# Kernel tuning notes

Measured on AMD Instinct MI355X. Metric: run time of the kernel, lower is better.

## Reference

```python
import jax, jax.numpy as jnp
import numpy as np

B, S, E, H = 2, 2048, 1024, 16
D = E // H  # head_dim
SCALE = 1.0 / np.sqrt(D)


def rope_tables(seq_len, dim, dtype=jnp.float32):
    # matches RotaryEmbedding: inv_freq over even indices, emb = cat([freqs, freqs])
    inv_freq = 1.0 / (10000.0 ** (jnp.arange(0, dim, 2, dtype=dtype) / dim))
    t = jnp.arange(seq_len, dtype=dtype)
    freqs = t[:, None] * inv_freq[None, :]          # [S, D/2]
    emb = jnp.concatenate([freqs, freqs], axis=-1)  # [S, D]
    return jnp.cos(emb)[None, None], jnp.sin(emb)[None, None]  # [1,1,S,D]


def apply_rope(x, cos, sin):
    # x: [B,H,S,D]; interleaved rotate exactly as the torch code:
    # x2 = stack([-x[...,1::2], x[...,0::2]], -1).reshape_as(x)
    x2 = jnp.stack([-x[..., 1::2], x[..., 0::2]], axis=-1).reshape(x.shape)
    return x * cos + x2 * sin


def setup_inputs() -> dict:
    key = jax.random.key(0)
    ks = jax.random.split(key, 12)
    std = 1.0 / np.sqrt(E)
    inp = {
        "query": jax.random.normal(ks[0], (B, S, E), jnp.float32),
        "key": jax.random.normal(ks[1], (B, S, E), jnp.float32),
        "value": jax.random.normal(ks[2], (B, S, E), jnp.float32),
        "mask": jnp.ones((B, S), jnp.int32),
        "Wq": jax.random.normal(ks[3], (E, E), jnp.float32) * std,
        "bq": jax.random.normal(ks[4], (E,), jnp.float32) * std,
        "Wk": jax.random.normal(ks[5], (E, E), jnp.float32) * std,
        "bk": jax.random.normal(ks[6], (E,), jnp.float32) * std,
        "Wv": jax.random.normal(ks[7], (E, E), jnp.float32) * std,
        "bv": jax.random.normal(ks[8], (E,), jnp.float32) * std,
        "Wo": jax.random.normal(ks[9], (E, E), jnp.float32) * std,
        "bo": jax.random.normal(ks[10], (E,), jnp.float32) * std,
    }
    return inp


def reference(query, key, value, mask, Wq, bq, Wk, bk, Wv, bv, Wo, bo):
    b, sq, _ = query.shape
    sk = key.shape[1]
    # linear projections (torch Linear: x @ W.T + b), split into heads [B,H,S,D]
    Q = (query @ Wq.T + bq).reshape(b, sq, H, D).transpose(0, 2, 1, 3)
    K = (key @ Wk.T + bk).reshape(b, sk, H, D).transpose(0, 2, 1, 3)
    V = (value @ Wv.T + bv).reshape(b, sk, H, D).transpose(0, 2, 1, 3)
    cos_q, sin_q = rope_tables(sq, D)
    cos_k, sin_k = rope_tables(sk, D)
    Q = apply_rope(Q, cos_q, sin_q)
    K = apply_rope(K, cos_k, sin_k)
    scores = jnp.einsum("bhqd,bhkd->bhqk", Q, K) * SCALE
    neg_inf = jnp.finfo(scores.dtype).min
    scores = jnp.where(mask[:, None, None, :] == 0, neg_inf, scores)
    attn = jax.nn.softmax(scores, axis=-1)
    # dropout omitted (deterministic reference / eval mode)
    out = jnp.einsum("bhqk,bhkd->bhqd", attn, V)
    out = out.transpose(0, 2, 1, 3).reshape(b, sq, E)
    return out @ Wo.T + bo
```

## Files before the change

### kernel.cpp

```cpp
#include <hip/hip_runtime.h>
#include <stdint.h>

typedef unsigned short u16;
typedef __bf16 bf16x8 __attribute__((ext_vector_type(8)));
typedef float f32x4 __attribute__((ext_vector_type(4)));
typedef float f32x2 __attribute__((ext_vector_type(2)));
typedef u16 u16x4v __attribute__((ext_vector_type(4)));

#define DI __device__ __forceinline__

constexpr int BB = 2, SS = 2048, EE = 1024, HH = 16, DD = 64;
constexpr int MROWS = BB * SS;
constexpr int KDIM = 1024, NDIM = 1024;

DI u16 f2bf(float f) {
  uint32_t u = __float_as_uint(f);
  return (u16)((u + 0x7FFFu + ((u >> 16) & 1u)) >> 16);
}
DI float bf2f(u16 h) { return __uint_as_float(((uint32_t)h) << 16); }

DI uint32_t cvtpk_bf16(float a, float b) {
  uint32_t r;
  asm("v_cvt_pk_bf16_f32 %0, %1, %2" : "=v"(r) : "v"(a), "v"(b));
  return r;
}

DI void cp16(const void* g, void* lds) {
  __builtin_amdgcn_global_load_lds((const __attribute__((address_space(1))) void*)g,
                                   (__attribute__((address_space(3))) void*)lds, 16, 0, 0);
}

DI f32x4 mfma16(bf16x8 a, bf16x8 b, f32x4 c) {
  return __builtin_amdgcn_mfma_f32_16x16x32_bf16(a, b, c, 0, 0, 0);
}

__global__ __launch_bounds__(256) void prep_cast(
    const float* __restrict__ q, const float* __restrict__ k, const float* __restrict__ v,
    const float* __restrict__ wq, const float* __restrict__ wk, const float* __restrict__ wv,
    const float* __restrict__ wo,
    u16* __restrict__ qb, u16* __restrict__ kb, u16* __restrict__ vb,
    u16* __restrict__ wqb, u16* __restrict__ wkb, u16* __restrict__ wvb,
    u16* __restrict__ wob) {
  constexpr size_t SZI = (size_t)MROWS * EE;
  constexpr size_t SZW = (size_t)EE * EE;
  const size_t g = ((size_t)blockIdx.x * 256 + threadIdx.x) * 4;
  const float* src; u16* dst; size_t o;
  if (g < SZI)          { src = q; dst = qb; o = g; }
  else if (g < 2 * SZI) { src = k; dst = kb; o = g - SZI; }
  else if (g < 3 * SZI) { src = v; dst = vb; o = g - 2 * SZI; }
  else {
    size_t t2 = g - 3 * SZI;
    int wi = (int)(t2 / SZW);
    o = t2 - (size_t)(wi < 4 ? wi : 3) * SZW;
    src = wi == 0 ? wq : wi == 1 ? wk : wi == 2 ? wv : wo;
    dst = wi == 0 ? wqb : wi == 1 ? wkb : wi == 2 ? wvb : wob;
  }
  const float4 f = *(const float4*)(src + o);
  u16x4v hv;
  hv[0] = f2bf(f.x); hv[1] = f2bf(f.y); hv[2] = f2bf(f.z); hv[3] = f2bf(f.w);
  *(u16x4v*)(dst + o) = hv;
}

__global__ __launch_bounds__(256) void rope_tables_k(float* __restrict__ csT) {
  const int t = blockIdx.x * 256 + threadIdx.x;
  const int s = t >> 6, d = t & 63, j = d & 31;
  const float ang = (float)s * exp2f(-(float)j * 0.4152410118f);
  float2 cs; cs.x = cosf(ang); cs.y = sinf(ang);
  ((float2*)csT)[t] = cs;
}

__global__ __launch_bounds__(256) void gemm_qkv(
    const u16* __restrict__ qb, const u16* __restrict__ kb, const u16* __restrict__ vb,
    const u16* __restrict__ wqb, const u16* __restrict__ wkb, const u16* __restrict__ wvb,
    const float* __restrict__ bq, const float* __restrict__ bk, const float* __restrict__ bv,
    u16* __restrict__ Qp, u16* __restrict__ Kp, u16* __restrict__ Vtg,
    const float* __restrict__ csT) {
  __shared__ alignas(16) u16 sA[128 * 64];
  __shared__ alignas(16) u16 sB[128 * 64];
  const int tsel = blockIdx.y >> 5;
  const bool vtr = (tsel == 2);
  const u16* A    = tsel == 0 ? wqb : tsel == 1 ? wkb : vb;
  const u16* Bm   = tsel == 0 ? qb  : tsel == 1 ? kb  : wvb;
  const float* bias = tsel == 0 ? bq : tsel == 1 ? bk : bv;

  const int fBase = blockIdx.x * 128;
  const int tBase = (blockIdx.y & 31) * 128;
  const int aBase = vtr ? tBase : fBase;
  const int bBase = vtr ? fBase : tBase;
  const int tid = threadIdx.x;
  const int lane = tid & 63, w = tid >> 6;
  const int quad = lane >> 4, l16 = lane & 15;
  const int wr = w >> 1, wc = w & 1;

  size_t aSrc[4], bSrc[4];
  u16 *aDst[4], *bDst[4];
#pragma unroll
  for (int j = 0; j < 4; ++j) {
    const int c = tid + j * 256;
    const int row = c >> 3, sl = c & 7;
    const size_t off = (size_t)row * KDIM + ((sl ^ (row & 7)) * 8);
    aSrc[j] = (size_t)aBase * KDIM + off; aDst[j] = &sA[c * 8];
    bSrc[j] = (size_t)bBase * KDIM + off; bDst[j] = &sB[c * 8];
  }

  f32x4 acc[4][4];
#pragma unroll
  for (int mi = 0; mi < 4; ++mi)
#pragma unroll
    for (int ni = 0; ni < 4; ++ni)
#pragma unroll
      for (int e = 0; e < 4; ++e) acc[mi][ni][e] = 0.f;

  const int arow = wr * 64 + l16, brow = wc * 64 + l16;

  for (int k0 = 0; k0 < KDIM; k0 += 64) {
    __syncthreads();
#pragma unroll
    for (int j = 0; j < 4; ++j) {
      cp16(A + aSrc[j] + k0, aDst[j]);
      cp16(Bm + bSrc[j] + k0, bDst[j]);
    }
    __syncthreads();
#pragma unroll
    for (int h = 0; h < 2; ++h) {
      bf16x8 af[4], bf[4];
#pragma unroll
      for (int i = 0; i < 4; ++i) {
        const int ar = arow + i * 16, br = brow + i * 16;
        af[i] = *(const bf16x8*)&sA[ar * 64 + (((h * 4 + quad) ^ (ar & 7)) << 3)];
        bf[i] = *(const bf16x8*)&sB[br * 64 + (((h * 4 + quad) ^ (br & 7)) << 3)];
      }
#pragma unroll
      for (int mi = 0; mi < 4; ++mi)
#pragma unroll
        for (int ni = 0; ni < 4; ++ni)
          acc[mi][ni] = mfma16(af[mi], bf[ni], acc[mi][ni]);
    }
  }

  if (!vtr) {
    u16* C = tsel == 0 ? Qp : Kp;
#pragma unroll
    for (int mi = 0; mi < 4; ++mi) {
      const int fm = fBase + wr * 64 + mi * 16 + quad * 4;
      const float4 b4 = *(const float4*)&bias[fm];
      const int d0 = fm & 63;
#pragma unroll
      for (int ni = 0; ni < 4; ++ni) {
        const int t = tBase + wc * 64 + ni * 16 + l16;
        const int srow = t & (SS - 1);
        const float* cs = &csT[(size_t)((srow << 6) + d0) * 2];
        const float4 cs01 = *(const float4*)cs;
        const float4 cs23 = *(const float4*)(cs + 4);
        const float v0 = acc[mi][ni][0] + b4.x;
        const float v1 = acc[mi][ni][1] + b4.y;
        const float v2 = acc[mi][ni][2] + b4.z;
        const float v3 = acc[mi][ni][3] + b4.w;
        const float o0 = v0 * cs01.x - v1 * cs01.y;
        const float o1 = v1 * cs01.z + v0 * cs01.w;
        const float o2 = v2 * cs23.x - v3 * cs23.y;
        const float o3 = v3 * cs23.z + v2 * cs23.w;
        uint2 pk;
        pk.x = cvtpk_bf16(o0, o1);
        pk.y = cvtpk_bf16(o2, o3);
        *(uint2*)&C[(size_t)t * NDIM + fm] = pk;
      }
    }
  } else {
#pragma unroll
    for (int ni = 0; ni < 4; ++ni) {
      const int f = fBase + wc * 64 + ni * 16 + l16;
      const int h = f >> 6, d = f & 63;
      const float bb = bias[f];
#pragma unroll
      for (int mi = 0; mi < 4; ++mi) {
        const int t0 = tBase + wr * 64 + mi * 16 + quad * 4;
        const int b = t0 >> 11, s0 = t0 & (SS - 1);
        const int sp0 = (s0 & ~31) | (((s0 >> 2) & 3) << 3) | (((s0 >> 4) & 1) << 2);
        uint2 pk;
        pk.x = cvtpk_bf16(acc[mi][ni][0] + bb, acc[mi][ni][1] + bb);
        pk.y = cvtpk_bf16(acc[mi][ni][2] + bb, acc[mi][ni][3] + bb);
        *(uint2*)&Vtg[((size_t)((b * 16 + h) * 64 + d)) * SS + sp0] = pk;
      }
    }
  }
}

__global__ __launch_bounds__(512, 4) void attn_kernel(
    const u16* __restrict__ Qp, const u16* __restrict__ Kp, const u16* __restrict__ Vtg,
    const int* __restrict__ mask, u16* __restrict__ Oh) {
  __shared__ alignas(16) u16 sK[128 * 64];
  __shared__ alignas(16) u16 sVt[64 * 128];
  __shared__ float sMask[128];
  const int tid = threadIdx.x, lane = tid & 63, w = tid >> 6;
  const int quad = lane >> 4, l16 = lane & 15;
  const int bh = blockIdx.y, b = bh >> 4, h = bh & 15;
  const int q0 = blockIdx.x * 128 + w * 16;
  const u16* Qb = Qp + (size_t)b * SS * EE + h * DD;
  const u16* Kb = Kp + (size_t)b * SS * EE + h * DD;
  const u16* Vb = Vtg + (size_t)bh * DD * SS;
  constexpr float C1 = 0.18033688011112042f;
  constexpr float FM = 12.0f;
  constexpr float MNEG = -30000.f;

  bf16x8 qf[2];
#pragma unroll
  for (int ks = 0; ks < 2; ++ks)
    qf[ks] = *(const bf16x8*)(Qb + (size_t)(q0 + l16) * EE + ks * 32 + quad * 8);

  f32x4 oacc[4];
#pragma unroll
  for (int nd = 0; nd < 4; ++nd)
#pragma unroll
    for (int e = 0; e < 4; ++e) oacc[nd][e] = 0.f;
  f32x2 sum2 = {0.f, 0.f};

  for (int kt = 0; kt < SS / 128; ++kt) {
    const int key0 = kt * 128;
    __syncthreads();
#pragma unroll
    for (int i = 0; i < 2; ++i) {
      const int c = i * 512 + tid;
      const int key = c >> 3;
      const int g8 = ((c & 7) ^ (key & 7)) * 8;
      cp16(Kb + (size_t)(key0 + key) * EE + g8, &sK[c * 8]);
    }
#pragma unroll
    for (int i = 0; i < 2; ++i) {
      const int L = i * 512 + tid;
      const int d = L >> 4;
      const int g8 = ((L & 15) ^ (d & 15)) * 8;
      cp16(Vb + (size_t)d * SS + key0 + g8, &sVt[L * 8]);
    }
    if (tid < 128) sMask[tid] = mask[b * SS + key0 + tid] ? -FM : MNEG;
    __syncthreads();

    f32x4 sacc[8];
#pragma unroll
    for (int ni = 0; ni < 8; ++ni)
#pragma unroll
      for (int e = 0; e < 4; ++e) sacc[ni][e] = 0.f;
#pragma unroll
    for (int ks = 0; ks < 2; ++ks)
#pragma unroll
      for (int ni = 0; ni < 8; ++ni) {
        const int row = ni * 16 + l16;
        const bf16x8 kf = *(const bf16x8*)&sK[row * 64 + (((ks * 4 + quad) ^ (l16 & 7)) << 3)];
        sacc[ni] = mfma16(kf, qf[ks], sacc[ni]);
      }

    uint32_t pw32[4][4];
#pragma unroll
    for (int ni = 0; ni < 8; ++ni) {
      const int kb4 = ni * 16 + quad * 4;
      const f32x2 m01 = *(const f32x2*)&sMask[kb4];
      const f32x2 m23 = *(const f32x2*)&sMask[kb4 + 2];
      f32x2 t01, t23;
      t01.x = sacc[ni][0]; t01.y = sacc[ni][1];
      t23.x = sacc[ni][2]; t23.y = sacc[ni][3];
      t01 = t01 * C1 + m01;
      t23 = t23 * C1 + m23;
      f32x2 p01, p23;
      p01.x = exp2f(t01.x); p01.y = exp2f(t01.y);
      p23.x = exp2f(t23.x); p23.y = exp2f(t23.y);
      sum2 += p01;
      sum2 += p23;
      const int k2 = ni >> 1, j2 = (ni & 1) * 2;
      pw32[k2][j2]     = cvtpk_bf16(p01.x, p01.y);
      pw32[k2][j2 + 1] = cvtpk_bf16(p23.x, p23.y);
    }

#pragma unroll
    for (int k2 = 0; k2 < 4; ++k2) {
      union { uint32_t u[4]; bf16x8 v; } pf;
#pragma unroll
      for (int j = 0; j < 4; ++j) pf.u[j] = pw32[k2][j];
#pragma unroll
      for (int nd = 0; nd < 4; ++nd) {
        const int row = nd * 16 + l16;
        const bf16x8 vf = *(const bf16x8*)&sVt[row * 128 + (((k2 * 4 + quad) ^ l16) << 3)];
        oacc[nd] = mfma16(pf.v, vf, oacc[nd]);
      }
    }
  }

  float lrow = sum2.x + sum2.y;
  lrow += __shfl_xor(lrow, 16, 64);
  lrow += __shfl_xor(lrow, 32, 64);
  const float linv = lrow > 0.f ? 1.0f / lrow : 0.f;

#pragma unroll
  for (int r = 0; r < 4; ++r) {
    const float li = __shfl(linv, quad * 4 + r, 16);
    const size_t row = (size_t)(b * SS + q0 + quad * 4 + r) * EE + h * DD;
#pragma unroll
    for (int nd = 0; nd < 4; ++nd) {
      const int d = nd * 16 + l16;
      Oh[row + d] = f2bf(oacc[nd][r] * li);
    }
  }
}

__global__ __launch_bounds__(256) void gemm_out(
    const u16* __restrict__ Ab, const u16* __restrict__ Bb,
    const float* __restrict__ bias, float* __restrict__ Cout) {
  __shared__ alignas(16) u16 sA[128 * 64];
  __shared__ alignas(16) u16 sB[64 * 64];
  const int rowBase = blockIdx.y * 128;
  const int colBase = blockIdx.x * 64;
  const int tid = threadIdx.x;
  const int lane = tid & 63, w = tid >> 6;
  const int quad = lane >> 4, l16 = lane & 15;
  const int wr = w >> 1, wc = w & 1;

  size_t aSrc[4]; u16* aDst[4];
  size_t bSrc[2]; u16* bDst[2];
#pragma unroll
  for (int j = 0; j < 4; ++j) {
    const int c = tid + j * 256;
    const int row = c >> 3, sl = c & 7;
    aSrc[j] = (size_t)(rowBase + row) * KDIM + ((sl ^ (row & 7)) * 8);
    aDst[j] = &sA[c * 8];
  }
#pragma unroll
  for (int j = 0; j < 2; ++j) {
    const int c = tid + j * 256;
    const int row = c >> 3, sl = c & 7;
    bSrc[j] = (size_t)(colBase + row) * KDIM + ((sl ^ (row & 7)) * 8);
    bDst[j] = &sB[c * 8];
  }

  f32x4 acc[4][2];
#pragma unroll
  for (int mi = 0; mi < 4; ++mi)
#pragma unroll
    for (int ni = 0; ni < 2; ++ni)
#pragma unroll
      for (int e = 0; e < 4; ++e) acc[mi][ni][e] = 0.f;

  const int arow = wr * 64 + l16, brow = wc * 32 + l16;

  for (int k0 = 0; k0 < KDIM; k0 += 64) {
    __syncthreads();
#pragma unroll
    for (int j = 0; j < 4; ++j) cp16(Ab + aSrc[j] + k0, aDst[j]);
#pragma unroll
    for (int j = 0; j < 2; ++j) cp16(Bb + bSrc[j] + k0, bDst[j]);
    __syncthreads();
#pragma unroll
    for (int h = 0; h < 2; ++h) {
      bf16x8 af[4], bf[2];
#pragma unroll
      for (int i = 0; i < 4; ++i) {
        const int ar = arow + i * 16;
        af[i] = *(const bf16x8*)&sA[ar * 64 + (((h * 4 + quad) ^ (ar & 7)) << 3)];
      }
#pragma unroll
      for (int i = 0; i < 2; ++i) {
        const int br = brow + i * 16;
        bf[i] = *(const bf16x8*)&sB[br * 64 + (((h * 4 + quad) ^ (br & 7)) << 3)];
      }
#pragma unroll
      for (int mi = 0; mi < 4; ++mi)
#pragma unroll
        for (int ni = 0; ni < 2; ++ni)
          acc[mi][ni] = mfma16(af[mi], bf[ni], acc[mi][ni]);
    }
  }

#pragma unroll
  for (int mi = 0; mi < 4; ++mi) {
    const int rb = rowBase + wr * 64 + mi * 16 + quad * 4;
#pragma unroll
    for (int ni = 0; ni < 2; ++ni) {
      const int col = colBase + wc * 32 + ni * 16 + l16;
      const float bb = bias[col];
#pragma unroll
      for (int r = 0; r < 4; ++r)
        Cout[(size_t)(rb + r) * NDIM + col] = acc[mi][ni][r] + bb;
    }
  }
}

extern "C" void kernel_launch(void* const* d_in, const int* in_sizes, int n_in,
                              void* d_out, int out_size, void* d_ws, size_t ws_size,
                              hipStream_t stream) {
  const float* q    = (const float*)d_in[0];
  const float* k    = (const float*)d_in[1];
  const float* v    = (const float*)d_in[2];
  const int*   mask = (const int*)d_in[3];
  const float* Wq = (const float*)d_in[4];
  const float* bq = (const float*)d_in[5];
  const float* Wk = (const float*)d_in[6];
  const float* bk = (const float*)d_in[7];
  const float* Wv = (const float*)d_in[8];
  const float* bv = (const float*)d_in[9];
  const float* Wo = (const float*)d_in[10];
  const float* bo = (const float*)d_in[11];
  float* out = (float*)d_out;
  char* ws = (char*)d_ws;
  constexpr size_t MB = 1024 * 1024;
  u16* qb  = (u16*)(ws + 0 * MB);
  u16* kb  = (u16*)(ws + 8 * MB);
  u16* vb  = (u16*)(ws + 16 * MB);
  u16* wqb = (u16*)(ws + 24 * MB);
  u16* wkb = (u16*)(ws + 26 * MB);
  u16* wvb = (u16*)(ws + 28 * MB);
  u16* wob = (u16*)(ws + 30 * MB);
  u16* Qp  = (u16*)(ws + 32 * MB);
  u16* Kp  = (u16*)(ws + 40 * MB);
  u16* Vtg = (u16*)(ws + 48 * MB);
  u16* oh  = (u16*)(ws + 56 * MB);
  float* csT = (float*)(ws + 64 * MB);

  prep_cast<<<16384, 256, 0, stream>>>(q, k, v, Wq, Wk, Wv, Wo,
                                       qb, kb, vb, wqb, wkb, wvb, wob);
  rope_tables_k<<<512, 256, 0, stream>>>(csT);
  gemm_qkv<<<dim3(8, 96), 256, 0, stream>>>(qb, kb, vb, wqb, wkb, wvb,
                                            bq, bk, bv, Qp, Kp, Vtg, csT);
  attn_kernel<<<dim3(16, 32), 512, 0, stream>>>(Qp, Kp, Vtg, mask, oh);
  gemm_out<<<dim3(16, 32), 256, 0, stream>>>(oh, wob, bo, out);
}
```

Measured before the change: 248.1 us.

## Double-buffer K/V tiles in attention and precompute mask bias once

Attention now double-buffers the K and V shared-memory tiles, so the async global-to-LDS loads for the next key tile overlap the MFMA and softmax work on the current one, with one barrier per tile instead of two. The mask-to-bias conversion moves into the rope-table kernel, written into the output buffer as scratch, and the whole mask row is loaded into LDS once per block. s_setprio raises wave priority around the MFMA sections. LDS use per block grows to roughly 72 KB, which may cut occupancy below the requested 4 blocks per CU.

```diff
diff --git a/kernel.cpp b/kernel.cpp
--- a/kernel.cpp
+++ b/kernel.cpp
@@ -12,6 +12,9 @@
 constexpr int BB = 2, SS = 2048, EE = 1024, HH = 16, DD = 64;
 constexpr int MROWS = BB * SS;
 constexpr int KDIM = 1024, NDIM = 1024;
+
+constexpr float FM = 12.0f;
+constexpr float MNEG = -30000.f;
 
 DI u16 f2bf(float f) {
   uint32_t u = __float_as_uint(f);
@@ -61,12 +64,15 @@
   *(u16x4v*)(dst + o) = hv;
 }
 
-__global__ __launch_bounds__(256) void rope_tables_k(float* __restrict__ csT) {
+__global__ __launch_bounds__(256) void rope_tables_k(float* __restrict__ csT,
+                                                     const int* __restrict__ mask,
+                                                     float* __restrict__ mfl) {
   const int t = blockIdx.x * 256 + threadIdx.x;
   const int s = t >> 6, d = t & 63, j = d & 31;
   const float ang = (float)s * exp2f(-(float)j * 0.4152410118f);
   float2 cs; cs.x = cosf(ang); cs.y = sinf(ang);
   ((float2*)csT)[t] = cs;
+  if (t < BB * SS) mfl[t] = mask[t] ? -FM : MNEG;
 }
 
 __global__ __launch_bounds__(256) void gemm_qkv(
@@ -188,10 +194,10 @@
 
 __global__ __launch_bounds__(512, 4) void attn_kernel(
     const u16* __restrict__ Qp, const u16* __restrict__ Kp, const u16* __restrict__ Vtg,
-    const int* __restrict__ mask, u16* __restrict__ Oh) {
-  __shared__ alignas(16) u16 sK[128 * 64];
-  __shared__ alignas(16) u16 sVt[64 * 128];
-  __shared__ float sMask[128];
+    const float* __restrict__ mfl, u16* __restrict__ Oh) {
+  __shared__ alignas(16) u16 sK[2][128 * 64];
+  __shared__ alignas(16) u16 sVt[2][64 * 128];
+  __shared__ alignas(16) float sMaskAll[SS];
   const int tid = threadIdx.x, lane = tid & 63, w = tid >> 6;
   const int quad = lane >> 4, l16 = lane & 15;
   const int bh = blockIdx.y, b = bh >> 4, h = bh & 15;
@@ -200,8 +206,6 @@
   const u16* Kb = Kp + (size_t)b * SS * EE + h * DD;
   const u16* Vb = Vtg + (size_t)bh * DD * SS;
   constexpr float C1 = 0.18033688011112042f;
-  constexpr float FM = 12.0f;
-  constexpr float MNEG = -30000.f;
 
   bf16x8 qf[2];
 #pragma unroll
@@ -215,46 +219,48 @@
     for (int e = 0; e < 4; ++e) oacc[nd][e] = 0.f;
   f32x2 sum2 = {0.f, 0.f};
 
-  for (int kt = 0; kt < SS / 128; ++kt) {
+  auto stage = [&](int kt, int bi) {
     const int key0 = kt * 128;
-    __syncthreads();
 #pragma unroll
     for (int i = 0; i < 2; ++i) {
       const int c = i * 512 + tid;
       const int key = c >> 3;
       const int g8 = ((c & 7) ^ (key & 7)) * 8;
-      cp16(Kb + (size_t)(key0 + key) * EE + g8, &sK[c * 8]);
+      cp16(Kb + (size_t)(key0 + key) * EE + g8, &sK[bi][c * 8]);
     }
 #pragma unroll
     for (int i = 0; i < 2; ++i) {
       const int L = i * 512 + tid;
       const int d = L >> 4;
       const int g8 = ((L & 15) ^ (d & 15)) * 8;
-      cp16(Vb + (size_t)d * SS + key0 + g8, &sVt[L * 8]);
-    }
-    if (tid < 128) sMask[tid] = mask[b * SS + key0 + tid] ? -FM : MNEG;
-    __syncthreads();
-
+      cp16(Vb + (size_t)d * SS + key0 + g8, &sVt[bi][L * 8]);
+    }
+  };
+
+  auto compute = [&](int kt, int bi) {
+    const int key0 = kt * 128;
     f32x4 sacc[8];
 #pragma unroll
     for (int ni = 0; ni < 8; ++ni)
 #pragma unroll
       for (int e = 0; e < 4; ++e) sacc[ni][e] = 0.f;
+    __builtin_amdgcn_s_setprio(1);
 #pragma unroll
     for (int ks = 0; ks < 2; ++ks)
 #pragma unroll
       for (int ni = 0; ni < 8; ++ni) {
         const int row = ni * 16 + l16;
-        const bf16x8 kf = *(const bf16x8*)&sK[row * 64 + (((ks * 4 + quad) ^ (l16 & 7)) << 3)];
+        const bf16x8 kf = *(const bf16x8*)&sK[bi][row * 64 + (((ks * 4 + quad) ^ (l16 & 7)) << 3)];
         sacc[ni] = mfma16(kf, qf[ks], sacc[ni]);
       }
+    __builtin_amdgcn_s_setprio(0);
 
     uint32_t pw32[4][4];
 #pragma unroll
     for (int ni = 0; ni < 8; ++ni) {
-      const int kb4 = ni * 16 + quad * 4;
-      const f32x2 m01 = *(const f32x2*)&sMask[kb4];
-      const f32x2 m23 = *(const f32x2*)&sMask[kb4 + 2];
+      const int kb4 = key0 + ni * 16 + quad * 4;
+      const f32x2 m01 = *(const f32x2*)&sMaskAll[kb4];
+      const f32x2 m23 = *(const f32x2*)&sMaskAll[kb4 + 2];
       f32x2 t01, t23;
       t01.x = sacc[ni][0]; t01.y = sacc[ni][1];
       t23.x = sacc[ni][2]; t23.y = sacc[ni][3];
@@ -270,6 +276,7 @@
       pw32[k2][j2 + 1] = cvtpk_bf16(p23.x, p23.y);
     }
 
+    __builtin_amdgcn_s_setprio(1);
 #pragma unroll
     for (int k2 = 0; k2 < 4; ++k2) {
       union { uint32_t u[4]; bf16x8 v; } pf;
@@ -278,10 +285,24 @@
 #pragma unroll
       for (int nd = 0; nd < 4; ++nd) {
         const int row = nd * 16 + l16;
-        const bf16x8 vf = *(const bf16x8*)&sVt[row * 128 + (((k2 * 4 + quad) ^ l16) << 3)];
+        const bf16x8 vf = *(const bf16x8*)&sVt[bi][row * 128 + (((k2 * 4 + quad) ^ l16) << 3)];
         oacc[nd] = mfma16(pf.v, vf, oacc[nd]);
       }
     }
+    __builtin_amdgcn_s_setprio(0);
+  };
+
+  stage(0, 0);
+  cp16(mfl + (size_t)b * SS + tid * 4, &sMaskAll[tid * 4]);
+  __syncthreads();
+
+  for (int kt = 0; kt < SS / 128; kt += 2) {
+    if (kt + 1 < SS / 128) stage(kt + 1, 1);
+    compute(kt, 0);
+    __syncthreads();
+    if (kt + 2 < SS / 128) stage(kt + 2, 0);
+    compute(kt + 1, 1);
+    __syncthreads();
   }
 
   float lrow = sum2.x + sum2.y;
@@ -412,12 +433,13 @@
   u16* Vtg = (u16*)(ws + 48 * MB);
   u16* oh  = (u16*)(ws + 56 * MB);
   float* csT = (float*)(ws + 64 * MB);
+  float* mfl = out;
 
   prep_cast<<<16384, 256, 0, stream>>>(q, k, v, Wq, Wk, Wv, Wo,
                                        qb, kb, vb, wqb, wkb, wvb, wob);
-  rope_tables_k<<<512, 256, 0, stream>>>(csT);
+  rope_tables_k<<<512, 256, 0, stream>>>(csT, mask, mfl);
   gemm_qkv<<<dim3(8, 96), 256, 0, stream>>>(qb, kb, vb, wqb, wkb, wvb,
                                             bq, bk, bv, Qp, Kp, Vtg, csT);
-  attn_kernel<<<dim3(16, 32), 512, 0, stream>>>(Qp, Kp, Vtg, mask, oh);
+  attn_kernel<<<dim3(16, 32), 512, 0, stream>>>(Qp, Kp, Vtg, mfl, oh);
   gemm_out<<<dim3(16, 32), 256, 0, stream>>>(oh, wob, bo, out);
 }
```

After: 250.4 us. Within noise of the previous version (+0.9%).
